# Kernel tuning notes

Hardware: AMD Instinct MI355X
Metric: run time of the kernel (lower is better)

The kernel has to match this reference:

```python
import jax, jax.numpy as jnp
import numpy as np
from jax import lax

B, S, T = 64, 50, 50
U, E = 1024, 256
VI, VT = 12000, 16000
BOS = 1


def _gru_step(h, x, Wx, Wh, b):
    # Keras GRU v2 (reset_after=True): b[0]=input bias, b[1]=recurrent bias
    gi = x @ Wx + b[0]          # [B, 3U]
    gh = h @ Wh + b[1]          # [B, 3U]
    iz, ir, ih = jnp.split(gi, 3, axis=-1)
    hz, hr, hh = jnp.split(gh, 3, axis=-1)
    z = jax.nn.sigmoid(iz + hz)
    r = jax.nn.sigmoid(ir + hr)
    hcand = jnp.tanh(ih + r * hh)
    return z * h + (1.0 - z) * hcand


def setup_inputs() -> dict:
    key = jax.random.key(0)
    ks = jax.random.split(key, 20)
    f = lambda k, shp: (jax.random.normal(k, shp, dtype=jnp.float32) * 0.05)
    inp = jax.random.randint(ks[0], (B, S), 0, VI)
    targ = jax.random.randint(ks[1], (B, T), 0, VT)
    targ = targ.at[:, 0].set(BOS)  # <bos> first token (teacher forcing input)
    return {
        'inp': inp,
        'targ': targ,
        'enc_hidden': jnp.zeros((B, U), jnp.float32),
        'enc_emb': f(ks[2], (VI, E)),
        'enc_Wx': f(ks[3], (E, 3 * U)),
        'enc_Wh': f(ks[4], (U, 3 * U)),
        'enc_b': jnp.zeros((2, 3 * U), jnp.float32),
        'W1': f(ks[5], (U, U)), 'b1': jnp.zeros((U,), jnp.float32),
        'W2': f(ks[6], (U, U)), 'b2': jnp.zeros((U,), jnp.float32),
        'V': f(ks[7], (U, 1)), 'bV': jnp.zeros((1,), jnp.float32),
        'dec_emb': f(ks[8], (VT, E)),
        'dec_Wx': f(ks[9], (U + E, 3 * U)),
        'dec_Wh': f(ks[10], (U, 3 * U)),
        'dec_b': jnp.zeros((2, 3 * U), jnp.float32),
        'fc_W': f(ks[11], (U, VT)), 'fc_b': jnp.zeros((VT,), jnp.float32),
    }


def reference(inp, targ, enc_hidden, enc_emb, enc_Wx, enc_Wh, enc_b,
              W1, b1, W2, b2, V, bV,
              dec_emb, dec_Wx, dec_Wh, dec_b, fc_W, fc_b):
    # ----- encoder GRU over source -----
    xe = enc_emb[inp]                             # [B,S,E]
    def enc_step(h, xt):
        h2 = _gru_step(h, xt, enc_Wx, enc_Wh, enc_b)
        return h2, h2
    h_last, outs = lax.scan(enc_step, enc_hidden, xe.transpose(1, 0, 2))
    enc_out = outs.transpose(1, 0, 2)             # [B,S,U]

    # ----- teacher-forcing decode -----
    keys = enc_out @ W2 + b2                      # W2(values), precomputed [B,S,U]
    dec_in_emb = dec_emb[targ[:, :-1]]            # [B,T-1,E] (col 0 is <bos>)
    targets = targ[:, 1:]                         # [B,T-1]

    def dec_step(dh, inps):
        x_emb, yt = inps                          # [B,E], [B]
        # Bahdanau attention on dec_hidden
        s = jnp.tanh((dh @ W1 + b1)[:, None, :] + keys)   # [B,S,U]
        score = jnp.einsum('bsu,uo->bso', s, V) + bV      # [B,S,1]
        attn = jax.nn.softmax(score, axis=1)
        ctx = jnp.sum(attn * enc_out, axis=1)             # [B,U]
        x = jnp.concatenate([ctx, x_emb], axis=-1)        # [B,U+E]
        # original code calls gru(x) with NO initial state -> zero h_prev
        h_new = _gru_step(jnp.zeros_like(dh), x, dec_Wx, dec_Wh, dec_b)
        logits = h_new @ fc_W + fc_b                      # [B,VT]
        logp = jax.nn.log_softmax(logits, axis=-1)
        nll = -jnp.take_along_axis(logp, yt[:, None], axis=1)[:, 0]
        mask = (yt != 0).astype(nll.dtype)
        return h_new, jnp.mean(nll * mask)

    _, losses = lax.scan(dec_step, h_last,
                         (dec_in_emb.transpose(1, 0, 2), targets.T))
    return jnp.sum(losses)
```

## Files before the change

### kernel.cpp

```cpp
#include <hip/hip_runtime.h>
#include <cstdint>
#include <cstddef>

#define BB 64
#define SS 50
#define TT 50
#define TD 49
#define UU 1024
#define EE 256
#define VT 16000
#define G3 3072
#define MPAD 3200

using short8 = __attribute__((ext_vector_type(8))) short;
using short4v = __attribute__((ext_vector_type(4))) short;
using uint4v = __attribute__((ext_vector_type(4))) unsigned int;
using f32x4  = __attribute__((ext_vector_type(4))) float;

__device__ __forceinline__ short f2bf(float f) {
    uint32_t u = __float_as_uint(f);
    uint32_t r = (u + 0x7fffu + ((u >> 16) & 1u)) >> 16;
    return (short)r;
}
__device__ __forceinline__ float bf2f(short s) {
    return __uint_as_float(((uint32_t)(uint16_t)s) << 16);
}
__device__ __forceinline__ float sigm(float x) { return 1.0f / (1.0f + __expf(-x)); }
__device__ __forceinline__ float ftanh(float x) {
    float xc = fminf(fmaxf(x, -8.0f), 8.0f);
    float e = __expf(2.0f * xc);
    return (e - 1.0f) / (e + 1.0f);
}

__device__ __forceinline__ short8 vload16(const short* p) {
    union { uint4v u; short8 s; } c;
    c.u = *(const volatile uint4v*)p;
    return c.s;
}
__device__ __forceinline__ float vload_bf(const short* p) { return bf2f(*(const volatile short*)p); }
__device__ __forceinline__ void vstore_bf(short* p, float v) { *(volatile short*)p = f2bf(v); }

__device__ __forceinline__ void gbar(int* flags, int* go, int t) {
    asm volatile("s_waitcnt vmcnt(0)" ::: "memory");
    __syncthreads();
    if (blockIdx.x == 0) {
        if (threadIdx.x < 64) {
            if (threadIdx.x == 0)
                __hip_atomic_store(&flags[0], t, __ATOMIC_RELAXED, __HIP_MEMORY_SCOPE_AGENT);
            int v;
            do {
                v = __hip_atomic_load(&flags[threadIdx.x], __ATOMIC_RELAXED, __HIP_MEMORY_SCOPE_AGENT);
            } while (__ballot(v >= t) != ~0ull);
            if (threadIdx.x == 0)
                __hip_atomic_store(go, t, __ATOMIC_RELAXED, __HIP_MEMORY_SCOPE_AGENT);
        }
    } else {
        if (threadIdx.x == 0) {
            __hip_atomic_store(&flags[blockIdx.x], t, __ATOMIC_RELAXED, __HIP_MEMORY_SCOPE_AGENT);
            while (__hip_atomic_load(go, __ATOMIC_RELAXED, __HIP_MEMORY_SCOPE_AGENT) < t)
                __builtin_amdgcn_s_sleep(1);
        }
    }
    __syncthreads();
}

typedef __attribute__((address_space(3))) void lds_vp;
typedef __attribute__((address_space(1))) void gl_vp;
__device__ __forceinline__ void gload16(void* lds, const void* g) {
    __builtin_amdgcn_global_load_lds((const gl_vp*)(uintptr_t)g,
                                     (lds_vp*)(uint32_t)(uintptr_t)lds,
                                     16, 0, 0);
}
__device__ __forceinline__ f32x4 mfma16(short8 a, short8 b, f32x4 c) {
    return __builtin_amdgcn_mfma_f32_16x16x32_bf16(a, b, c, 0, 0, 0);
}

template<int BM, int BN, int WM, int WN, bool OUT_BF16, int REMAP>
__global__ __launch_bounds__(256) void gemm_bf16(
    const short* __restrict__ A, const short* __restrict__ Bt,
    const float* __restrict__ bias, void* __restrict__ C, int N, int K,
    int lda, int ldb)
{
    constexpr int BK = 32;
    __shared__ __attribute__((aligned(16))) short As[BM * BK];
    __shared__ __attribute__((aligned(16))) short Bs[BN * BK];

    const int tid  = threadIdx.x;
    const int wave = tid >> 6;
    const int lane = tid & 63;
    const int l15  = lane & 15;
    const int quad = lane >> 4;
    const int wm = wave >> 1, wn = wave & 1;
    const int n0 = blockIdx.x * BN;
    const int m0 = blockIdx.y * BM;

    f32x4 acc[WM / 16][WN / 16];
    #pragma unroll
    for (int i = 0; i < WM / 16; ++i)
        #pragma unroll
        for (int j = 0; j < WN / 16; ++j)
            acc[i][j] = (f32x4)0.0f;

    for (int k0 = 0; k0 < K; k0 += BK) {
        #pragma unroll
        for (int it = 0; it < BM / 64; ++it) {
            int e = (it * 256 + tid) * 8;
            int row = e >> 5, col = e & 31;
            gload16(As + (it * 256 + wave * 64) * 8,
                    A + (size_t)(m0 + row) * lda + k0 + col);
        }
        #pragma unroll
        for (int it = 0; it < BN / 64; ++it) {
            int e = (it * 256 + tid) * 8;
            int row = e >> 5, col = e & 31;
            gload16(Bs + (it * 256 + wave * 64) * 8,
                    Bt + (size_t)(n0 + row) * ldb + k0 + col);
        }
        __syncthreads();
        short8 af[WM / 16], bfr[WN / 16];
        #pragma unroll
        for (int i = 0; i < WM / 16; ++i)
            af[i] = *(const short8*)(As + (wm * WM + i * 16 + l15) * BK + quad * 8);
        #pragma unroll
        for (int j = 0; j < WN / 16; ++j)
            bfr[j] = *(const short8*)(Bs + (wn * WN + j * 16 + l15) * BK + quad * 8);
        #pragma unroll
        for (int i = 0; i < WM / 16; ++i)
            #pragma unroll
            for (int j = 0; j < WN / 16; ++j)
                acc[i][j] = mfma16(af[i], bfr[j], acc[i][j]);
        __syncthreads();
    }

    #pragma unroll
    for (int i = 0; i < WM / 16; ++i) {
        #pragma unroll
        for (int j = 0; j < WN / 16; ++j) {
            int row = m0 + wm * WM + i * 16 + quad * 4;
            int col = n0 + wn * WN + j * 16 + l15;
            float bia = bias ? bias[col] : 0.0f;
            #pragma unroll
            for (int r = 0; r < 4; ++r) {
                size_t off;
                if (REMAP == 1)
                    off = ((size_t)((row + r) & 63) * SS + ((row + r) >> 6)) * N + col;
                else if (REMAP == 2)
                    off = (((size_t)((row + r) & 63) * SS + ((row + r) >> 6)) * UU
                           + (col & 1023)) * 4 + (col >> 10);
                else
                    off = (size_t)(row + r) * N + col;
                float v = acc[i][j][r] + bia;
                if (OUT_BF16) ((short*)C)[off] = f2bf(v);
                else          ((float*)C)[off] = v;
            }
        }
    }
}

__global__ __launch_bounds__(256) void transpose_bf(
    const float* __restrict__ in, short* __restrict__ out, int ldin, int ldout)
{
    __shared__ float tile[64][65];
    int n0 = blockIdx.x * 64, k0 = blockIdx.y * 64;
    int c = threadIdx.x & 63, rr = threadIdx.x >> 6;
    #pragma unroll 4
    for (int i = 0; i < 16; ++i) {
        int row = rr * 16 + i;
        tile[row][c] = in[(size_t)(k0 + row) * ldin + n0 + c];
    }
    __syncthreads();
    #pragma unroll 4
    for (int i = 0; i < 16; ++i) {
        int row = rr * 16 + i;
        out[(size_t)(n0 + row) * ldout + k0 + c] = f2bf(tile[c][row]);
    }
}

__global__ __launch_bounds__(256) void transpose_pack(
    const float* __restrict__ W, short* __restrict__ Wp, int N, int K)
{
    int lane = threadIdx.x & 63;
    int it = blockIdx.x * 4 + (threadIdx.x >> 6);
    int nt = blockIdx.y;
    int KI = K >> 5;
    int kb = it * 32 + (lane >> 4) * 8;
    int n  = nt * 16 + (lane & 15);
    short8 v;
    #pragma unroll
    for (int e = 0; e < 8; ++e)
        v[e] = f2bf(W[(size_t)(kb + e) * N + n]);
    *(short8*)(Wp + (((size_t)nt * KI + it) * 64 + lane) * 8) = v;
}

__global__ __launch_bounds__(256) void prep_gather(
    const int* __restrict__ inp, const int* __restrict__ targ,
    const float* __restrict__ enc_emb, const float* __restrict__ dec_emb,
    const float* __restrict__ enc_h0,
    short* __restrict__ Ae, short* __restrict__ Ad,
    short* __restrict__ H_bf, short* __restrict__ h0_bf,
    float* __restrict__ out, int* __restrict__ bar)
{
    int blk = blockIdx.x, tid = threadIdx.x;
    if (blk < MPAD) {
        int s = blk >> 6, b = blk & 63;
        int row = inp[b * SS + s];
        Ae[(size_t)blk * EE + tid] = f2bf(enc_emb[(size_t)row * EE + tid]);
    } else if (blk < 2 * MPAD) {
        int m = blk - MPAD;
        if (m < TD * BB) {
            int t = m >> 6, b = m & 63;
            int row = targ[b * TT + t];
            Ad[(size_t)m * EE + tid] = f2bf(dec_emb[(size_t)row * EE + tid]);
        } else {
            Ad[(size_t)m * EE + tid] = 0;
        }
    } else {
        int r = blk - 2 * MPAD;
        for (int u = tid; u < UU; u += 256) {
            H_bf[(size_t)(TD * BB + r) * UU + u] = 0;
            h0_bf[(size_t)r * UU + u] = f2bf(enc_h0[(size_t)r * UU + u]);
        }
        if (r == 0) {
            bar[tid] = 0;
            if (tid == 0) out[0] = 0.0f;
        }
    }
}

__global__ __launch_bounds__(1024) void enc_scan(
    const short* __restrict__ h0, const short* __restrict__ Whp,
    const short* __restrict__ gi, const float* __restrict__ bias2,
    short* __restrict__ eout, int* __restrict__ bar)
{
    const int j    = blockIdx.x;
    const int tid  = threadIdx.x;
    const int lane = tid & 63;
    const int l15  = lane & 15;
    const int quad = lane >> 4;
    const int wave = tid >> 6;
    const int bg   = wave & 3;
    const int kq   = wave >> 2;
    const int u    = j * 16 + l15;

    __shared__ f32x4 red[4][3][4][64];
    int* flags = bar;     int* go = bar + 64;

    const short* Bp0 = Whp + ((((size_t)(0 * 64 + j)) * 32 + kq * 8) * 64 + lane) * 8;
    const short* Bp1 = Whp + ((((size_t)(1 * 64 + j)) * 32 + kq * 8) * 64 + lane) * 8;
    const short* Bp2 = Whp + ((((size_t)(2 * 64 + j)) * 32 + kq * 8) * 64 + lane) * 8;
    const float bz = bias2[u], br = bias2[UU + u], bh = bias2[2 * UU + u];

    for (int t = 0; t < SS; ++t) {
        const short* A = t ? eout + (size_t)(t - 1) * BB * UU : h0;
        const short* Arow = A + (size_t)(bg * 16 + l15) * UU + kq * 256 + quad * 8;
        f32x4 a0 = (f32x4)0.0f, a1 = (f32x4)0.0f, a2 = (f32x4)0.0f;
        #pragma unroll
        for (int i = 0; i < 8; ++i) {
            short8 af = vload16(Arow + i * 32);
            a0 = mfma16(af, *(const short8*)(Bp0 + i * 512), a0);
            a1 = mfma16(af, *(const short8*)(Bp1 + i * 512), a1);
            a2 = mfma16(af, *(const short8*)(Bp2 + i * 512), a2);
        }
        red[kq][0][bg][lane] = a0;
        red[kq][1][bg][lane] = a1;
        red[kq][2][bg][lane] = a2;
        __syncthreads();
        if (kq == 0) {
            f32x4 s0 = red[0][0][bg][lane] + red[1][0][bg][lane] + red[2][0][bg][lane] + red[3][0][bg][lane];
            f32x4 s1 = red[0][1][bg][lane] + red[1][1][bg][lane] + red[2][1][bg][lane] + red[3][1][bg][lane];
            f32x4 s2 = red[0][2][bg][lane] + red[1][2][bg][lane] + red[2][2][bg][lane] + red[3][2][bg][lane];
            const short* git = gi + (size_t)t * BB * G3;
            #pragma unroll
            for (int r = 0; r < 4; ++r) {
                int b = bg * 16 + quad * 4 + r;
                const short* gb = git + (size_t)b * G3;
                float iz = bf2f(gb[u]), ir = bf2f(gb[UU + u]), ih = bf2f(gb[2 * UU + u]);
                float h = vload_bf(A + (size_t)b * UU + u);
                float z  = sigm(iz + s0[r] + bz);
                float rr = sigm(ir + s1[r] + br);
                float hc = ftanh(ih + rr * (s2[r] + bh));
                vstore_bf(eout + (size_t)t * BB * UU + (size_t)b * UU + u,
                          z * h + (1.0f - z) * hc);
            }
        }
        if (t != SS - 1) gbar(flags, go, t + 1);
    }
}

__global__ __launch_bounds__(1024) void dec_scan(
    const short* __restrict__ eout, const short* __restrict__ W1p,
    const float* __restrict__ b1, const short* __restrict__ keyp,
    const float* __restrict__ Vw, const float* __restrict__ bV,
    const short* __restrict__ Pp4, const short* __restrict__ xg,
    const float* __restrict__ db1, short* __restrict__ q_bf,
    short* __restrict__ Hbf, int* __restrict__ bar)
{
    const int j    = blockIdx.x;
    const int tid  = threadIdx.x;
    const int lane = tid & 63;
    const int l15  = lane & 15;
    const int quad = lane >> 4;
    const int wave = tid >> 6;
    const int bg   = wave & 3;
    const int kq   = wave >> 2;
    const int u    = j * 16 + l15;

    __shared__ f32x4 redq[4][4][64];
    __shared__ float sc[64];
    __shared__ float attnw[64];
    int* flags = bar + 128;  int* go = bar + 192;

    const short* BpQ = W1p + (((size_t)j * 32 + kq * 8) * 64 + lane) * 8;
    const float b1v = b1[u];
    const float bV0 = bV[0];

    float Vl[16];
    #pragma unroll
    for (int e = 0; e < 16; e += 4)
        *(float4*)&Vl[e] = *(const float4*)(Vw + lane * 16 + e);

    const float dz3 = db1[tid], dr3 = db1[UU + tid], dh3 = db1[2 * UU + tid];
    const short* Pb = Pp4 + (size_t)j * SS * UU * 4;

    for (int t = 0; t < TD; ++t) {
        const short* dh = t ? Hbf + (size_t)(t - 1) * BB * UU
                            : eout + (size_t)(SS - 1) * BB * UU;
        {
            const short* Arow = dh + (size_t)(bg * 16 + l15) * UU + kq * 256 + quad * 8;
            f32x4 aq = (f32x4)0.0f;
            #pragma unroll
            for (int i = 0; i < 8; ++i)
                aq = mfma16(vload16(Arow + i * 32), *(const short8*)(BpQ + i * 512), aq);
            redq[kq][bg][lane] = aq;
        }
        __syncthreads();
        if (kq == 0) {
            f32x4 s = redq[0][bg][lane] + redq[1][bg][lane] + redq[2][bg][lane] + redq[3][bg][lane];
            #pragma unroll
            for (int r = 0; r < 4; ++r)
                vstore_bf(q_bf + (size_t)(bg * 16 + quad * 4 + r) * UU + u, s[r] + b1v);
        }
        gbar(flags, go, 2 * t + 1);
        {
            const int b = j;
            float ql[16];
            {
                short8 q0 = vload16(q_bf + (size_t)b * UU + lane * 16);
                short8 q1 = vload16(q_bf + (size_t)b * UU + lane * 16 + 8);
                #pragma unroll
                for (int e = 0; e < 8; ++e) { ql[e] = bf2f(q0[e]); ql[8 + e] = bf2f(q1[e]); }
            }
            for (int s = wave; s < SS; s += 16) {
                const short* kp = keyp + ((size_t)b * SS + s) * UU + lane * 16;
                short8 k0 = *(const short8*)kp;
                short8 k1 = *(const short8*)(kp + 8);
                float p = 0.0f;
                #pragma unroll
                for (int e = 0; e < 8; ++e) p += Vl[e] * ftanh(ql[e] + bf2f(k0[e]));
                #pragma unroll
                for (int e = 0; e < 8; ++e) p += Vl[8 + e] * ftanh(ql[8 + e] + bf2f(k1[e]));
                #pragma unroll
                for (int off = 32; off; off >>= 1) p += __shfl_down(p, off);
                if (lane == 0) sc[s] = p + bV0;
            }
            __syncthreads();
            if (wave == 0) {
                float v = (lane < SS) ? sc[lane] : -1e30f;
                float m = v;
                #pragma unroll
                for (int off = 32; off; off >>= 1) m = fmaxf(m, __shfl_down(m, off));
                m = __shfl(m, 0);
                float e = (lane < SS) ? __expf(v - m) : 0.0f;
                float ss = e;
                #pragma unroll
                for (int off = 32; off; off >>= 1) ss += __shfl_down(ss, off);
                ss = __shfl(ss, 0);
                if (lane < SS) attnw[lane] = e / ss;
            }
            __syncthreads();
            float g0 = 0.0f, g1 = 0.0f, g2 = 0.0f;
            const short* Pu = Pb + (size_t)tid * 4;
            #pragma unroll 2
            for (int s = 0; s < SS; ++s) {
                float w = attnw[s];
                short4v pv = *(const short4v*)(Pu + (size_t)s * UU * 4);
                g0 += w * bf2f(pv[0]);
                g1 += w * bf2f(pv[1]);
                g2 += w * bf2f(pv[2]);
            }
            const short* xb = xg + ((size_t)t * BB + b) * G3;
            g0 += bf2f(xb[tid]);
            g1 += bf2f(xb[UU + tid]);
            g2 += bf2f(xb[2 * UU + tid]);
            float z  = sigm(g0 + dz3);
            float rr = sigm(g1 + dr3);
            float hc = ftanh(g2 + rr * dh3);
            vstore_bf(Hbf + ((size_t)t * BB + b) * UU + tid, (1.0f - z) * hc);
        }
        if (t != TD - 1) gbar(flags, go, 2 * t + 2);
    }
}

__global__ __launch_bounds__(256) void loss_kernel(
    const float* __restrict__ logits, const int* __restrict__ targ,
    int rows0, float* __restrict__ out)
{
    int gr = rows0 + blockIdx.x;
    int t = gr >> 6;
    if (t >= TD) return;
    int b = gr & 63;
    const float* lp = logits + (size_t)blockIdx.x * VT;
    int tid = threadIdx.x;
    __shared__ float redm[4], reds[4];

    float m = -INFINITY;
    for (int v = tid; v < VT; v += 256) m = fmaxf(m, lp[v]);
    #pragma unroll
    for (int off = 32; off; off >>= 1) m = fmaxf(m, __shfl_down(m, off));
    if ((tid & 63) == 0) redm[tid >> 6] = m;
    __syncthreads();
    float mm = fmaxf(fmaxf(redm[0], redm[1]), fmaxf(redm[2], redm[3]));

    float ssum = 0.0f;
    for (int v = tid; v < VT; v += 256) ssum += expf(lp[v] - mm);
    #pragma unroll
    for (int off = 32; off; off >>= 1) ssum += __shfl_down(ssum, off);
    if ((tid & 63) == 0) reds[tid >> 6] = ssum;
    __syncthreads();
    if (tid == 0) {
        float tot = reds[0] + reds[1] + reds[2] + reds[3];
        int y = targ[b * TT + t + 1];
        float nll = mm + logf(tot) - lp[y];
        if (y != 0) atomicAdd(out, nll * (1.0f / (float)BB));
    }
}

extern "C" void kernel_launch(void* const* d_in, const int* in_sizes, int n_in,
                              void* d_out, int out_size, void* d_ws, size_t ws_size,
                              hipStream_t stream)
{
    (void)in_sizes; (void)n_in; (void)out_size;
    const int*   inp      = (const int*)  d_in[0];
    const int*   targ     = (const int*)  d_in[1];
    const float* enc_h0   = (const float*)d_in[2];
    const float* enc_emb  = (const float*)d_in[3];
    const float* enc_Wx   = (const float*)d_in[4];
    const float* enc_Wh   = (const float*)d_in[5];
    const float* enc_b    = (const float*)d_in[6];
    const float* W1       = (const float*)d_in[7];
    const float* b1       = (const float*)d_in[8];
    const float* W2       = (const float*)d_in[9];
    const float* b2       = (const float*)d_in[10];
    const float* Vw       = (const float*)d_in[11];
    const float* bV       = (const float*)d_in[12];
    const float* dec_emb  = (const float*)d_in[13];
    const float* dec_Wx   = (const float*)d_in[14];
    const float* dec_b    = (const float*)d_in[16];
    const float* fc_W     = (const float*)d_in[17];
    const float* fc_b     = (const float*)d_in[18];
    float* out = (float*)d_out;

    char* p = (char*)d_ws;
    auto alloc = [&](size_t bytes) {
        char* r = (char*)(((uintptr_t)p + 255) & ~(uintptr_t)255);
        p = r + bytes;
        return r;
    };
    short* encWxt  = (short*)alloc((size_t)G3 * EE * 2);
    short* W2t     = (short*)alloc((size_t)UU * UU * 2);
    short* dWxt_c  = (short*)alloc((size_t)G3 * UU * 2);
    short* dWxt_e  = (short*)alloc((size_t)G3 * EE * 2);
    short* fcWt    = (short*)alloc((size_t)VT * UU * 2);
    short* encWhp  = (short*)alloc((size_t)G3 * UU * 2);
    short* W1p     = (short*)alloc((size_t)UU * UU * 2);
    short* Ae      = (short*)alloc((size_t)MPAD * EE * 2);
    short* Ad      = (short*)alloc((size_t)MPAD * EE * 2);
    short* enc_gi  = (short*)alloc((size_t)MPAD * G3 * 2);
    short* xemb_gi = (short*)alloc((size_t)MPAD * G3 * 2);
    short* enc_out = (short*)alloc((size_t)MPAD * UU * 2);
    short* keyp    = (short*)alloc((size_t)MPAD * UU * 2);
    short* Pp4     = (short*)alloc((size_t)MPAD * UU * 4 * 2);
    short* H_bf    = (short*)alloc((size_t)MPAD * UU * 2);
    short* h0_bf   = (short*)alloc((size_t)BB * UU * 2);
    short* q_bf    = (short*)alloc((size_t)BB * UU * 2);
    int*   bar     = (int*)alloc(256 * 4);

    size_t used = (size_t)(p - (char*)d_ws);
    size_t avail = (ws_size > used) ? ws_size - used : 0;
    int chunkRows = 640;
    while (chunkRows > 128 && (size_t)chunkRows * VT * 4 + 4096 > avail) chunkRows -= 128;
    float* logits = (float*)alloc((size_t)chunkRows * VT * 4);

    transpose_bf<<<dim3(G3/64, EE/64), 256, 0, stream>>>(enc_Wx, encWxt, G3, EE);
    transpose_bf<<<dim3(UU/64, UU/64), 256, 0, stream>>>(W2, W2t, UU, UU);
    transpose_bf<<<dim3(G3/64, UU/64), 256, 0, stream>>>(dec_Wx, dWxt_c, G3, UU);
    transpose_bf<<<dim3(G3/64, EE/64), 256, 0, stream>>>(dec_Wx + (size_t)UU * G3, dWxt_e, G3, EE);
    transpose_bf<<<dim3(VT/64, UU/64), 256, 0, stream>>>(fc_W, fcWt, VT, UU);
    transpose_pack<<<dim3(8, G3/16), 256, 0, stream>>>(enc_Wh, encWhp, G3, UU);
    transpose_pack<<<dim3(8, UU/16), 256, 0, stream>>>(W1, W1p, UU, UU);
    prep_gather<<<2 * MPAD + 64, 256, 0, stream>>>(inp, targ, enc_emb, dec_emb, enc_h0,
                                                   Ae, Ad, H_bf, h0_bf, out, bar);

    gemm_bf16<128,128,64,64,true,0><<<dim3(G3/128, MPAD/128), 256, 0, stream>>>(
        Ae, encWxt, enc_b, enc_gi, G3, EE, EE, EE);
    gemm_bf16<128,128,64,64,true,0><<<dim3(G3/128, MPAD/128), 256, 0, stream>>>(
        Ad, dWxt_e, dec_b, xemb_gi, G3, EE, EE, EE);

    {
        const short* a0 = h0_bf; const short* a1 = encWhp; const short* a2 = enc_gi;
        const float* a3 = enc_b + G3; short* a4 = enc_out; int* a5 = bar;
        void* args[] = {&a0, &a1, &a2, &a3, &a4, &a5};
        hipLaunchCooperativeKernel((void*)enc_scan, dim3(64), dim3(1024), args, 0, stream);
    }

    gemm_bf16<128,128,64,64,true,1><<<dim3(UU/128, MPAD/128), 256, 0, stream>>>(
        enc_out, W2t, b2, keyp, UU, UU, UU, UU);
    gemm_bf16<128,128,64,64,true,2><<<dim3(G3/128, MPAD/128), 256, 0, stream>>>(
        enc_out, dWxt_c, nullptr, Pp4, G3, UU, UU, UU);

    {
        const short* a0 = enc_out; const short* a1 = W1p; const float* a2 = b1;
        const short* a3 = keyp; const float* a4 = Vw; const float* a5 = bV;
        const short* a6 = Pp4; const short* a7 = xemb_gi; const float* a8 = dec_b + G3;
        short* a9 = q_bf; short* a10 = H_bf; int* a11 = bar;
        void* args[] = {&a0, &a1, &a2, &a3, &a4, &a5, &a6, &a7, &a8, &a9, &a10, &a11};
        hipLaunchCooperativeKernel((void*)dec_scan, dim3(64), dim3(1024), args, 0, stream);
    }

    for (int rows0 = 0; rows0 < MPAD; rows0 += chunkRows) {
        int rows = MPAD - rows0; if (rows > chunkRows) rows = chunkRows;
        gemm_bf16<128,128,64,64,false,0><<<dim3(VT/128, rows/128), 256, 0, stream>>>(
            H_bf + (size_t)rows0 * UU, fcWt, fc_b, logits, VT, UU, UU, UU);
        loss_kernel<<<rows, 256, 0, stream>>>(logits, targ, rows0, out);
    }
}
```

Measured before the change: 2.702 ms.

## Use all-to-all flag barrier and batch loads in encoder/decoder scans

Replaces the two-phase grid barrier, where block 0 gathers flags and then releases a go flag, with a symmetric barrier in which every block polls all 64 flags. This removes one round-trip of global-memory latency per step. The encoder and decoder scans also issue all A-fragment and gate loads before the MFMA and elementwise math, and the decoder stages its W1 slice in LDS once at kernel start. The attention-context loop gets a deeper unroll. The cost is more polling traffic across all blocks and extra registers and LDS.

```diff
diff --git a/kernel.cpp b/kernel.cpp
--- a/kernel.cpp
+++ b/kernel.cpp
@@ -40,26 +40,17 @@
 __device__ __forceinline__ float vload_bf(const short* p) { return bf2f(*(const volatile short*)p); }
 __device__ __forceinline__ void vstore_bf(short* p, float v) { *(volatile short*)p = f2bf(v); }
 
-__device__ __forceinline__ void gbar(int* flags, int* go, int t) {
+__device__ __forceinline__ void gbar(int* flags, int t) {
     asm volatile("s_waitcnt vmcnt(0)" ::: "memory");
     __syncthreads();
-    if (blockIdx.x == 0) {
-        if (threadIdx.x < 64) {
-            if (threadIdx.x == 0)
-                __hip_atomic_store(&flags[0], t, __ATOMIC_RELAXED, __HIP_MEMORY_SCOPE_AGENT);
-            int v;
-            do {
-                v = __hip_atomic_load(&flags[threadIdx.x], __ATOMIC_RELAXED, __HIP_MEMORY_SCOPE_AGENT);
-            } while (__ballot(v >= t) != ~0ull);
-            if (threadIdx.x == 0)
-                __hip_atomic_store(go, t, __ATOMIC_RELAXED, __HIP_MEMORY_SCOPE_AGENT);
-        }
-    } else {
-        if (threadIdx.x == 0) {
+    if (threadIdx.x < 64) {
+        if (threadIdx.x == 0)
             __hip_atomic_store(&flags[blockIdx.x], t, __ATOMIC_RELAXED, __HIP_MEMORY_SCOPE_AGENT);
-            while (__hip_atomic_load(go, __ATOMIC_RELAXED, __HIP_MEMORY_SCOPE_AGENT) < t)
-                __builtin_amdgcn_s_sleep(1);
-        }
+        asm volatile("" ::: "memory");
+        int v;
+        do {
+            v = __hip_atomic_load(&flags[threadIdx.x], __ATOMIC_RELAXED, __HIP_MEMORY_SCOPE_AGENT);
+        } while (__ballot(v >= t) != ~0ull);
     }
     __syncthreads();
 }
@@ -243,7 +234,7 @@
     const int u    = j * 16 + l15;
 
     __shared__ f32x4 red[4][3][4][64];
-    int* flags = bar;     int* go = bar + 64;
+    int* flags = bar;
 
     const short* Bp0 = Whp + ((((size_t)(0 * 64 + j)) * 32 + kq * 8) * 64 + lane) * 8;
     const short* Bp1 = Whp + ((((size_t)(1 * 64 + j)) * 32 + kq * 8) * 64 + lane) * 8;
@@ -253,13 +244,15 @@
     for (int t = 0; t < SS; ++t) {
         const short* A = t ? eout + (size_t)(t - 1) * BB * UU : h0;
         const short* Arow = A + (size_t)(bg * 16 + l15) * UU + kq * 256 + quad * 8;
+        short8 af[8];
+        #pragma unroll
+        for (int i = 0; i < 8; ++i) af[i] = vload16(Arow + i * 32);
         f32x4 a0 = (f32x4)0.0f, a1 = (f32x4)0.0f, a2 = (f32x4)0.0f;
         #pragma unroll
         for (int i = 0; i < 8; ++i) {
-            short8 af = vload16(Arow + i * 32);
-            a0 = mfma16(af, *(const short8*)(Bp0 + i * 512), a0);
-            a1 = mfma16(af, *(const short8*)(Bp1 + i * 512), a1);
-            a2 = mfma16(af, *(const short8*)(Bp2 + i * 512), a2);
+            a0 = mfma16(af[i], *(const short8*)(Bp0 + i * 512), a0);
+            a1 = mfma16(af[i], *(const short8*)(Bp1 + i * 512), a1);
+            a2 = mfma16(af[i], *(const short8*)(Bp2 + i * 512), a2);
         }
         red[kq][0][bg][lane] = a0;
         red[kq][1][bg][lane] = a1;
@@ -270,20 +263,31 @@
             f32x4 s1 = red[0][1][bg][lane] + red[1][1][bg][lane] + red[2][1][bg][lane] + red[3][1][bg][lane];
             f32x4 s2 = red[0][2][bg][lane] + red[1][2][bg][lane] + red[2][2][bg][lane] + red[3][2][bg][lane];
             const short* git = gi + (size_t)t * BB * G3;
+            float hv[4], izv[4], irv[4], ihv[4];
+            #pragma unroll
+            for (int r = 0; r < 4; ++r) {
+                int b = bg * 16 + quad * 4 + r;
+                hv[r] = vload_bf(A + (size_t)b * UU + u);
+            }
             #pragma unroll
             for (int r = 0; r < 4; ++r) {
                 int b = bg * 16 + quad * 4 + r;
                 const short* gb = git + (size_t)b * G3;
-                float iz = bf2f(gb[u]), ir = bf2f(gb[UU + u]), ih = bf2f(gb[2 * UU + u]);
-                float h = vload_bf(A + (size_t)b * UU + u);
-                float z  = sigm(iz + s0[r] + bz);
-                float rr = sigm(ir + s1[r] + br);
-                float hc = ftanh(ih + rr * (s2[r] + bh));
+                izv[r] = bf2f(gb[u]);
+                irv[r] = bf2f(gb[UU + u]);
+                ihv[r] = bf2f(gb[2 * UU + u]);
+            }
+            #pragma unroll
+            for (int r = 0; r < 4; ++r) {
+                int b = bg * 16 + quad * 4 + r;
+                float z  = sigm(izv[r] + s0[r] + bz);
+                float rr = sigm(irv[r] + s1[r] + br);
+                float hc = ftanh(ihv[r] + rr * (s2[r] + bh));
                 vstore_bf(eout + (size_t)t * BB * UU + (size_t)b * UU + u,
-                          z * h + (1.0f - z) * hc);
-            }
-        }
-        if (t != SS - 1) gbar(flags, go, t + 1);
+                          z * hv[r] + (1.0f - z) * hc);
+            }
+        }
+        if (t != SS - 1) gbar(flags, t + 1);
     }
 }
 
@@ -308,9 +312,20 @@
     __shared__ f32x4 redq[4][4][64];
     __shared__ float sc[64];
     __shared__ float attnw[64];
-    int* flags = bar + 128;  int* go = bar + 192;
-
-    const short* BpQ = W1p + (((size_t)j * 32 + kq * 8) * 64 + lane) * 8;
+    __shared__ __attribute__((aligned(16))) short Ws[32 * 512];
+    int* flags = bar + 128;
+
+    {
+        const short* src = W1p + (size_t)j * 32 * 512;
+        #pragma unroll
+        for (int it2 = 0; it2 < 2; ++it2) {
+            int cb = it2 * 1024 + wave * 64;
+            gload16(Ws + (size_t)cb * 8, src + (size_t)(cb + lane) * 8);
+        }
+        __syncthreads();
+    }
+
+    const short* BpL = Ws + ((size_t)kq * 8) * 512 + (size_t)lane * 8;
     const float b1v = b1[u];
     const float bV0 = bV[0];
 
@@ -327,10 +342,13 @@
                             : eout + (size_t)(SS - 1) * BB * UU;
         {
             const short* Arow = dh + (size_t)(bg * 16 + l15) * UU + kq * 256 + quad * 8;
+            short8 af[8];
+            #pragma unroll
+            for (int i = 0; i < 8; ++i) af[i] = vload16(Arow + i * 32);
             f32x4 aq = (f32x4)0.0f;
             #pragma unroll
             for (int i = 0; i < 8; ++i)
-                aq = mfma16(vload16(Arow + i * 32), *(const short8*)(BpQ + i * 512), aq);
+                aq = mfma16(af[i], *(const short8*)(BpL + i * 512), aq);
             redq[kq][bg][lane] = aq;
         }
         __syncthreads();
@@ -340,7 +358,7 @@
             for (int r = 0; r < 4; ++r)
                 vstore_bf(q_bf + (size_t)(bg * 16 + quad * 4 + r) * UU + u, s[r] + b1v);
         }
-        gbar(flags, go, 2 * t + 1);
+        gbar(flags, 2 * t + 1);
         {
             const int b = j;
             float ql[16];
@@ -378,9 +396,12 @@
                 if (lane < SS) attnw[lane] = e / ss;
             }
             __syncthreads();
-            float g0 = 0.0f, g1 = 0.0f, g2 = 0.0f;
+            const short* xb = xg + ((size_t)t * BB + b) * G3;
+            float g0 = bf2f(xb[tid]);
+            float g1 = bf2f(xb[UU + tid]);
+            float g2 = bf2f(xb[2 * UU + tid]);
             const short* Pu = Pb + (size_t)tid * 4;
-            #pragma unroll 2
+            #pragma unroll 10
             for (int s = 0; s < SS; ++s) {
                 float w = attnw[s];
                 short4v pv = *(const short4v*)(Pu + (size_t)s * UU * 4);
@@ -388,16 +409,12 @@
                 g1 += w * bf2f(pv[1]);
                 g2 += w * bf2f(pv[2]);
             }
-            const short* xb = xg + ((size_t)t * BB + b) * G3;
-            g0 += bf2f(xb[tid]);
-            g1 += bf2f(xb[UU + tid]);
-            g2 += bf2f(xb[2 * UU + tid]);
             float z  = sigm(g0 + dz3);
             float rr = sigm(g1 + dr3);
             float hc = ftanh(g2 + rr * dh3);
             vstore_bf(Hbf + ((size_t)t * BB + b) * UU + tid, (1.0f - z) * hc);
         }
-        if (t != TD - 1) gbar(flags, go, 2 * t + 2);
+        if (t != TD - 1) gbar(flags, 2 * t + 2);
     }
 }
 
```

Result: slower. 2.862 ms (+5.9%).
